# Optimization experiments

Hardware: AMD Instinct MI355X
Metric: run time of the kernel (lower is better)

## Reference

```python
import jax, jax.numpy as jnp
import numpy as np

N_CHANNELS = 1024
N_HEADS = 16
BLOCK_SIZE = 2048
BATCH = 4
SEQ = 2048


def setup_inputs() -> dict:
    key = jax.random.key(0)
    k_x, k_wqkv, k_wproj = jax.random.split(key, 3)
    x = jax.random.normal(k_x, (BATCH, SEQ, N_CHANNELS), dtype=jnp.float32)
    # torch nn.Linear: y = x @ W.T + b, W shape [out, in], init normal(std=0.02)
    W_qkv = jax.random.normal(k_wqkv, (3 * N_CHANNELS, N_CHANNELS), dtype=jnp.float32) * 0.02
    b_qkv = jnp.zeros((3 * N_CHANNELS,), dtype=jnp.float32)
    W_proj = jax.random.normal(k_wproj, (N_CHANNELS, N_CHANNELS), dtype=jnp.float32) * 0.02
    b_proj = jnp.zeros((N_CHANNELS,), dtype=jnp.float32)
    return {"x": x, "W_qkv": W_qkv, "b_qkv": b_qkv, "W_proj": W_proj, "b_proj": b_proj}


def reference(x, W_qkv, b_qkv, W_proj, b_proj):
    bs, n, n_channels = x.shape
    n_heads = N_HEADS
    head_dim = n_channels // n_heads
    scale = head_dim ** (-0.5)

    qkv = x @ W_qkv.T + b_qkv                              # [b, n, 3C]
    qkv = qkv.reshape(bs, n, 3, n_heads, head_dim)
    q, k, v = qkv[:, :, 0], qkv[:, :, 1], qkv[:, :, 2]     # [b, n, h, d]

    logits = jnp.einsum('bthc,bshc->bhts', q, k) * scale   # [b, h, t, s]
    # causal mask: log(tril(ones)) = 0 below diagonal, -inf above
    causal = jnp.tril(jnp.ones((n, n), dtype=bool))
    logits = jnp.where(causal[None, None], logits, -jnp.inf)
    attn = jax.nn.softmax(logits, axis=-1)

    output = jnp.einsum('bhts,bshc->bthc', attn, v)        # [b, t, h, d]
    output = output.reshape(bs, n, n_channels)
    output = output @ W_proj.T + b_proj
    return output
```

## Files before the change

kernel.cpp:

```cpp
#include <hip/hip_runtime.h>
#include <hip/hip_bf16.h>
#include <stdint.h>

#define BATCH 4
#define SEQ   2048
#define NC    1024
#define NH    16
#define HD    64
#define NT    16

typedef __bf16 bf16x8 __attribute__((ext_vector_type(8)));
typedef __bf16 bf16x2 __attribute__((ext_vector_type(2)));
typedef float  f32x4  __attribute__((ext_vector_type(4)));
typedef float  f32x16 __attribute__((ext_vector_type(16)));

#define DEV __device__ __forceinline__

DEV unsigned short f2bf(float f) {
    union { float f; unsigned u; } v; v.f = f;
    unsigned r = (v.u + 0x7fffu + ((v.u >> 16) & 1u)) >> 16;
    return (unsigned short)r;
}

DEV float fast_exp2(float x) {
#if __has_builtin(__builtin_amdgcn_exp2f)
    return __builtin_amdgcn_exp2f(x);
#else
    return exp2f(x);
#endif
}

DEV void plane32_swap(uint32_t& a, uint32_t& b) {
#if __has_builtin(__builtin_amdgcn_permlane32_swap)
    auto r = __builtin_amdgcn_permlane32_swap(a, b, false, false);
    a = (uint32_t)r[0];
    b = (uint32_t)r[1];
#else
    uint32_t sa = __shfl_xor(a, 32), sb = __shfl_xor(b, 32);
    const bool hi = ((threadIdx.x & 63) >= 32);
    uint32_t na = hi ? sb : a;
    uint32_t nb = hi ? b : sa;
    a = na; b = nb;
#endif
}

#define GLDS16(gsrc, ldst)                                                           \
    __builtin_amdgcn_global_load_lds(                                                \
        (const __attribute__((address_space(1))) unsigned int*)(gsrc),               \
        (__attribute__((address_space(3))) unsigned int*)(ldst), 16, 0, 0)

__global__ void cvt_kernel(const float* __restrict__ in, unsigned short* __restrict__ out, int n4) {
    int i = blockIdx.x * 256 + threadIdx.x;
    if (i >= n4) return;
    float4 v = reinterpret_cast<const float4*>(in)[i];
    ushort4 o;
    o.x = f2bf(v.x); o.y = f2bf(v.y); o.z = f2bf(v.z); o.w = f2bf(v.w);
    reinterpret_cast<ushort4*>(out)[i] = o;
}

template <bool BF16_OUT>
__global__ __launch_bounds__(256, 2) void gemm_bt_kernel(
    const unsigned short* __restrict__ A,
    const unsigned short* __restrict__ W,
    const float* __restrict__ bias,
    void* __restrict__ Cout,
    int M, int N, int K, int scale_n, float scale)
{
    __shared__ __align__(16) char Alds[128 * 128];
    __shared__ __align__(16) char Blds[128 * 128];

    const int tid = threadIdx.x;
    const int w = tid >> 6, l = tid & 63, g = l >> 4, lr = l & 15;
    const int nt = N >> 7;
    const int cpx = gridDim.x >> 3;
    const int bid = (blockIdx.x & 7) * cpx + (blockIdx.x >> 3);
    const int mtile = bid / nt, ntile = bid % nt;
    const int m0 = mtile << 7, n0 = ntile << 7;
    const int wr = (w >> 1) << 6, wc = (w & 1) << 6;

    f32x4 acc[4][4] = {};

    for (int kt = 0; kt < K; kt += 64) {
        if (kt) __syncthreads();
#pragma unroll
        for (int i = 0; i < 4; ++i) {
            const int issue = (i << 2) + w;
            const int row = (issue << 3) + (l >> 3);
            const int chunk = (l & 7) ^ (row & 7);
            GLDS16((const char*)(A + (size_t)(m0 + row) * K + kt) + (chunk << 4),
                   Alds + (issue << 10));
        }
#pragma unroll
        for (int i = 0; i < 4; ++i) {
            const int issue = (i << 2) + w;
            const int row = (issue << 3) + (l >> 3);
            const int chunk = (l & 7) ^ (row & 7);
            GLDS16((const char*)(W + (size_t)(n0 + row) * K + kt) + (chunk << 4),
                   Blds + (issue << 10));
        }
        __syncthreads();

#pragma unroll
        for (int kb = 0; kb < 2; ++kb) {
            bf16x8 af[4], bfr[4];
#pragma unroll
            for (int mf = 0; mf < 4; ++mf) {
                const int row = wr + (mf << 4) + lr;
                const int chunk = ((kb << 2) + g) ^ (row & 7);
                af[mf] = *reinterpret_cast<const bf16x8*>(Alds + row * 128 + (chunk << 4));
            }
#pragma unroll
            for (int nf = 0; nf < 4; ++nf) {
                const int row = wc + (nf << 4) + lr;
                const int chunk = ((kb << 2) + g) ^ (row & 7);
                bfr[nf] = *reinterpret_cast<const bf16x8*>(Blds + row * 128 + (chunk << 4));
            }
#pragma unroll
            for (int mf = 0; mf < 4; ++mf)
#pragma unroll
                for (int nf = 0; nf < 4; ++nf)
                    acc[mf][nf] = __builtin_amdgcn_mfma_f32_16x16x32_bf16(
                        af[mf], bfr[nf], acc[mf][nf], 0, 0, 0);
        }
    }

#pragma unroll
    for (int mf = 0; mf < 4; ++mf) {
#pragma unroll
        for (int nf = 0; nf < 4; ++nf) {
            const int n = n0 + wc + (nf << 4) + lr;
            const float bscale = (n < scale_n) ? scale : 1.0f;
            const float bv = bias[n];
#pragma unroll
            for (int r = 0; r < 4; ++r) {
                const int m = m0 + wr + (mf << 4) + (g << 2) + r;
                float v2 = (acc[mf][nf][r] + bv) * bscale;
                if (BF16_OUT)
                    ((unsigned short*)Cout)[(size_t)m * N + n] = f2bf(v2);
                else
                    ((float*)Cout)[(size_t)m * N + n] = v2;
            }
        }
    }
}

__global__ __launch_bounds__(256, 4) void attn_kernel(
    const unsigned short* __restrict__ qkv,
    unsigned short* __restrict__ ctx)
{
    __shared__ __align__(16) char Klds[2][8192];
    __shared__ __align__(16) char Vt[2][64 * 144];

    const int tid = threadIdx.x;
    const int w = tid >> 6, l = tid & 63, hi = l >> 5, lq = l & 31;
    const int bid = blockIdx.x;
    const int qt = NT - 1 - (bid >> 6);
    const int h = (bid >> 2) & 15, b = bid & 3;
    const unsigned short* base = qkv + (size_t)b * SEQ * 3072 + h * 64;

    const int vkey0 = (tid >> 5) << 3;
    const int vd0   = (tid & 31) << 1;
    const unsigned short* vbase = base + 2048 + (size_t)vkey0 * 3072 + vd0;

    const int q0 = (qt << 7) + (w << 5);
    const int q = q0 + lq;
    const int ntiles = (qt + 1) << 1;

    bf16x8 qfr[4];
#pragma unroll
    for (int ds = 0; ds < 4; ++ds)
        qfr[ds] = *reinterpret_cast<const bf16x8*>(
            base + (size_t)q * 3072 + (ds << 4) + (hi << 3));

    f32x16 acc0 = {}, acc1 = {};
    float mrun = -INFINITY, lrun = 0.f;

    uint32_t vreg[8];

#pragma unroll
    for (int i = 0; i < 8; ++i)
        vreg[i] = *reinterpret_cast<const uint32_t*>(vbase + (size_t)i * 3072);
#pragma unroll
    for (int i = 0; i < 2; ++i) {
        const int issue = (i << 2) + w;
        const int row = (issue << 3) + (l >> 3);
        const int chunk = (l & 7) ^ (row & 7);
        GLDS16((const char*)(base + 1024 + (size_t)row * 3072) + (chunk << 4),
               Klds[0] + (issue << 10));
    }
    {
        uint4 a, bq;
        a.x = (vreg[0] & 0xffffu) | (vreg[1] << 16);
        a.y = (vreg[2] & 0xffffu) | (vreg[3] << 16);
        a.z = (vreg[4] & 0xffffu) | (vreg[5] << 16);
        a.w = (vreg[6] & 0xffffu) | (vreg[7] << 16);
        bq.x = (vreg[0] >> 16) | (vreg[1] & 0xffff0000u);
        bq.y = (vreg[2] >> 16) | (vreg[3] & 0xffff0000u);
        bq.z = (vreg[4] >> 16) | (vreg[5] & 0xffff0000u);
        bq.w = (vreg[6] >> 16) | (vreg[7] & 0xffff0000u);
        *reinterpret_cast<uint4*>(Vt[0] + vd0 * 144 + vkey0 * 2) = a;
        *reinterpret_cast<uint4*>(Vt[0] + (vd0 + 1) * 144 + vkey0 * 2) = bq;
    }
    __syncthreads();

    for (int t = 0; t < ntiles; ++t) {
        const int cur = t & 1;
        const int kv0 = t << 6;
        const bool pf_ = (t + 1 < ntiles);

        if (pf_) {
            const int kv1 = kv0 + 64;
#pragma unroll
            for (int i = 0; i < 8; ++i)
                vreg[i] = *reinterpret_cast<const uint32_t*>(
                    vbase + (size_t)(kv1 + i) * 3072);
#pragma unroll
            for (int i = 0; i < 2; ++i) {
                const int issue = (i << 2) + w;
                const int row = (issue << 3) + (l >> 3);
                const int chunk = (l & 7) ^ (row & 7);
                GLDS16((const char*)(base + 1024 + (size_t)(kv1 + row) * 3072) + (chunk << 4),
                       Klds[cur ^ 1] + (issue << 10));
            }
        }

        if (kv0 <= q0 + 31) {
            const bool do1 = (kv0 + 32 <= q0 + 31);

            f32x16 st0 = {}, st1 = {};
#pragma unroll
            for (int ds = 0; ds < 4; ++ds) {
                const int chunk = (((ds << 1) + hi) ^ (lq & 7)) << 4;
                bf16x8 k0 = *reinterpret_cast<const bf16x8*>(
                    Klds[cur] + lq * 128 + chunk);
                st0 = __builtin_amdgcn_mfma_f32_32x32x16_bf16(k0, qfr[ds], st0, 0, 0, 0);
            }
            if (do1) {
#pragma unroll
                for (int ds = 0; ds < 4; ++ds) {
                    const int chunk = (((ds << 1) + hi) ^ (lq & 7)) << 4;
                    bf16x8 k1 = *reinterpret_cast<const bf16x8*>(
                        Klds[cur] + (lq + 32) * 128 + chunk);
                    st1 = __builtin_amdgcn_mfma_f32_32x32x16_bf16(k1, qfr[ds], st1, 0, 0, 0);
                }
            }

            if (kv0 + 31 > q0) {
#pragma unroll
                for (int r = 0; r < 16; ++r) {
                    const int key = kv0 + ((r & 3) + ((r >> 2) << 3) + (hi << 2));
                    if (key > q) st0[r] = -INFINITY;
                }
            }
            if (do1 && kv0 + 63 > q0) {
#pragma unroll
                for (int r = 0; r < 16; ++r) {
                    const int key = kv0 + 32 + ((r & 3) + ((r >> 2) << 3) + (hi << 2));
                    if (key > q) st1[r] = -INFINITY;
                }
            }

            float mt = st0[0];
#pragma unroll
            for (int r = 1; r < 16; ++r) mt = fmaxf(mt, st0[r]);
            if (do1) {
#pragma unroll
                for (int r = 0; r < 16; ++r) mt = fmaxf(mt, st1[r]);
            }
            mt = fmaxf(mt, __shfl_xor(mt, 32));
            if (__any(mt > mrun + 8.0f)) {
                const float mnew = fmaxf(mrun, mt);
                const float corr = fast_exp2(mrun - mnew);
                mrun = mnew;
                lrun *= corr;
#pragma unroll
                for (int r = 0; r < 16; ++r) { acc0[r] *= corr; acc1[r] *= corr; }
            }
            float rs = 0.f;
#pragma unroll
            for (int r = 0; r < 16; ++r) { st0[r] = fast_exp2(st0[r] - mrun); rs += st0[r]; }
            if (do1) {
#pragma unroll
                for (int r = 0; r < 16; ++r) { st1[r] = fast_exp2(st1[r] - mrun); rs += st1[r]; }
            }
            rs += __shfl_xor(rs, 32);
            lrun += rs;

            uint32_t pk0[8], pk1[8];
#pragma unroll
            for (int s = 0; s < 4; ++s)
#pragma unroll
                for (int c = 0; c < 2; ++c) {
                    bf16x2 t0 = {(__bf16)st0[(s << 2) + (c << 1)],
                                 (__bf16)st0[(s << 2) + (c << 1) + 1]};
                    pk0[(s << 1) + c] = __builtin_bit_cast(uint32_t, t0);
                }
            if (do1) {
#pragma unroll
                for (int s = 0; s < 4; ++s)
#pragma unroll
                    for (int c = 0; c < 2; ++c) {
                        bf16x2 t1 = {(__bf16)st1[(s << 2) + (c << 1)],
                                     (__bf16)st1[(s << 2) + (c << 1) + 1]};
                        pk1[(s << 1) + c] = __builtin_bit_cast(uint32_t, t1);
                    }
            }

            const int nkt = do1 ? 4 : 2;
#pragma unroll
            for (int kt = 0; kt < 4; ++kt) {
                if (kt >= nkt) break;
                const int s0 = (kt & 1) << 1;
                uint32_t x0, x1, y0, y1;
                if (kt < 2) {
                    x0 = pk0[(s0 << 1) + 0]; x1 = pk0[(s0 << 1) + 1];
                    y0 = pk0[(s0 << 1) + 2]; y1 = pk0[(s0 << 1) + 3];
                } else {
                    x0 = pk1[(s0 << 1) + 0]; x1 = pk1[(s0 << 1) + 1];
                    y0 = pk1[(s0 << 1) + 2]; y1 = pk1[(s0 << 1) + 3];
                }
                plane32_swap(x0, y0);
                plane32_swap(x1, y1);
                union { uint32_t u[4]; bf16x8 v; } pf;
                pf.u[0] = x0; pf.u[1] = x1; pf.u[2] = y0; pf.u[3] = y1;

                const char* vrow = Vt[cur] + ((kt << 4) + (hi << 3)) * 2;
                bf16x8 vf0 = *reinterpret_cast<const bf16x8*>(vrow + lq * 144);
                bf16x8 vf1 = *reinterpret_cast<const bf16x8*>(vrow + (lq + 32) * 144);
                acc0 = __builtin_amdgcn_mfma_f32_32x32x16_bf16(vf0, pf.v, acc0, 0, 0, 0);
                acc1 = __builtin_amdgcn_mfma_f32_32x32x16_bf16(vf1, pf.v, acc1, 0, 0, 0);
            }
        }

        if (pf_) {
            uint4 a, bq;
            a.x = (vreg[0] & 0xffffu) | (vreg[1] << 16);
            a.y = (vreg[2] & 0xffffu) | (vreg[3] << 16);
            a.z = (vreg[4] & 0xffffu) | (vreg[5] << 16);
            a.w = (vreg[6] & 0xffffu) | (vreg[7] << 16);
            bq.x = (vreg[0] >> 16) | (vreg[1] & 0xffff0000u);
            bq.y = (vreg[2] >> 16) | (vreg[3] & 0xffff0000u);
            bq.z = (vreg[4] >> 16) | (vreg[5] & 0xffff0000u);
            bq.w = (vreg[6] >> 16) | (vreg[7] & 0xffff0000u);
            char* vt = Vt[cur ^ 1];
            *reinterpret_cast<uint4*>(vt + vd0 * 144 + vkey0 * 2) = a;
            *reinterpret_cast<uint4*>(vt + (vd0 + 1) * 144 + vkey0 * 2) = bq;
            __syncthreads();
        }
    }

    {
        const float li = 1.0f / lrun;
        unsigned short* op = ctx + (size_t)(b * SEQ + q) * NC + h * HD;
#pragma unroll
        for (int r = 0; r < 16; ++r) {
            const int d = (r & 3) + ((r >> 2) << 3) + (hi << 2);
            op[d] = f2bf(acc0[r] * li);
            op[d + 32] = f2bf(acc1[r] * li);
        }
    }
}

extern "C" void kernel_launch(void* const* d_in, const int* in_sizes, int n_in,
                              void* d_out, int out_size, void* d_ws, size_t ws_size,
                              hipStream_t stream) {
    const float* x     = (const float*)d_in[0];
    const float* Wqkv  = (const float*)d_in[1];
    const float* bqkv  = (const float*)d_in[2];
    const float* Wproj = (const float*)d_in[3];
    const float* bproj = (const float*)d_in[4];
    float* out = (float*)d_out;

    const int M = BATCH * SEQ;
    unsigned short* ws = (unsigned short*)d_ws;
    unsigned short* xb     = ws;
    unsigned short* wqkvb  = xb + (size_t)M * NC;
    unsigned short* wprojb = wqkvb + (size_t)3 * NC * NC;
    unsigned short* qkvb   = wprojb + (size_t)NC * NC;
    unsigned short* ctxb   = qkvb + (size_t)M * 3 * NC;

    {
        int n4 = M * NC / 4;
        cvt_kernel<<<(n4 + 255) / 256, 256, 0, stream>>>(x, xb, n4);
    }
    {
        int n4 = 3 * NC * NC / 4;
        cvt_kernel<<<(n4 + 255) / 256, 256, 0, stream>>>(Wqkv, wqkvb, n4);
    }
    {
        int n4 = NC * NC / 4;
        cvt_kernel<<<(n4 + 255) / 256, 256, 0, stream>>>(Wproj, wprojb, n4);
    }

    gemm_bt_kernel<true><<<(M / 128) * (3 * NC / 128), 256, 0, stream>>>(
        xb, wqkvb, bqkv, qkvb, M, 3 * NC, NC, NC, 0.18033688011112042f);

    attn_kernel<<<NT * NH * BATCH, 256, 0, stream>>>(qkvb, ctxb);

    gemm_bt_kernel<false><<<(M / 128) * (NC / 128), 256, 0, stream>>>(
        ctxb, wprojb, bproj, out, M, NC, NC, 0, 1.0f);
}
```

Baseline: 158.8 us.

## Swizzle transposed V in LDS, snake query-tile order, add MFMA priority hints

The transposed V tile in LDS moves from a padded 144-byte row stride to a 128-byte stride with XOR swizzling of 16-byte chunks. This cuts LDS use and is meant to avoid bank conflicts on both the transpose writes and the MFMA operand reads. Block-to-query-tile mapping becomes a serpentine order across groups of four tiles, to balance causal work across waves of blocks. s_setprio raises wave priority around the QK and PV MFMA sections so matrix instructions issue ahead of other waves.

```diff
diff --git a/kernel.cpp b/kernel.cpp
--- a/kernel.cpp
+++ b/kernel.cpp
@@ -149,17 +149,20 @@
     unsigned short* __restrict__ ctx)
 {
     __shared__ __align__(16) char Klds[2][8192];
-    __shared__ __align__(16) char Vt[2][64 * 144];
+    __shared__ __align__(16) char Vt[2][8192];
 
     const int tid = threadIdx.x;
     const int w = tid >> 6, l = tid & 63, hi = l >> 5, lq = l & 31;
     const int bid = blockIdx.x;
-    const int qt = NT - 1 - (bid >> 6);
-    const int h = (bid >> 2) & 15, b = bid & 3;
+    const int s = bid >> 8, u = (bid >> 6) & 3, r0 = bid & 63;
+    const int v = (s & 1) ? 3 - u : u;
+    const int qt = NT - 1 - (s << 2) - v;
+    const int h = r0 >> 2, b = r0 & 3;
     const unsigned short* base = qkv + (size_t)b * SEQ * 3072 + h * 64;
 
     const int vkey0 = (tid >> 5) << 3;
     const int vd0   = (tid & 31) << 1;
+    const int vcc0  = vkey0 >> 3;
     const unsigned short* vbase = base + 2048 + (size_t)vkey0 * 3072 + vd0;
 
     const int q0 = (qt << 7) + (w << 5);
@@ -198,8 +201,10 @@
         bq.y = (vreg[2] >> 16) | (vreg[3] & 0xffff0000u);
         bq.z = (vreg[4] >> 16) | (vreg[5] & 0xffff0000u);
         bq.w = (vreg[6] >> 16) | (vreg[7] & 0xffff0000u);
-        *reinterpret_cast<uint4*>(Vt[0] + vd0 * 144 + vkey0 * 2) = a;
-        *reinterpret_cast<uint4*>(Vt[0] + (vd0 + 1) * 144 + vkey0 * 2) = bq;
+        *reinterpret_cast<uint4*>(
+            Vt[0] + vd0 * 128 + ((vcc0 ^ (vd0 & 7)) << 4)) = a;
+        *reinterpret_cast<uint4*>(
+            Vt[0] + (vd0 + 1) * 128 + ((vcc0 ^ ((vd0 + 1) & 7)) << 4)) = bq;
     }
     __syncthreads();
 
@@ -228,6 +233,7 @@
             const bool do1 = (kv0 + 32 <= q0 + 31);
 
             f32x16 st0 = {}, st1 = {};
+            __builtin_amdgcn_s_setprio(1);
 #pragma unroll
             for (int ds = 0; ds < 4; ++ds) {
                 const int chunk = (((ds << 1) + hi) ^ (lq & 7)) << 4;
@@ -244,6 +250,7 @@
                     st1 = __builtin_amdgcn_mfma_f32_32x32x16_bf16(k1, qfr[ds], st1, 0, 0, 0);
                 }
             }
+            __builtin_amdgcn_s_setprio(0);
 
             if (kv0 + 31 > q0) {
 #pragma unroll
@@ -288,25 +295,26 @@
 
             uint32_t pk0[8], pk1[8];
 #pragma unroll
-            for (int s = 0; s < 4; ++s)
+            for (int sp = 0; sp < 4; ++sp)
 #pragma unroll
                 for (int c = 0; c < 2; ++c) {
-                    bf16x2 t0 = {(__bf16)st0[(s << 2) + (c << 1)],
-                                 (__bf16)st0[(s << 2) + (c << 1) + 1]};
-                    pk0[(s << 1) + c] = __builtin_bit_cast(uint32_t, t0);
+                    bf16x2 t0 = {(__bf16)st0[(sp << 2) + (c << 1)],
+                                 (__bf16)st0[(sp << 2) + (c << 1) + 1]};
+                    pk0[(sp << 1) + c] = __builtin_bit_cast(uint32_t, t0);
                 }
             if (do1) {
 #pragma unroll
-                for (int s = 0; s < 4; ++s)
+                for (int sp = 0; sp < 4; ++sp)
 #pragma unroll
                     for (int c = 0; c < 2; ++c) {
-                        bf16x2 t1 = {(__bf16)st1[(s << 2) + (c << 1)],
-                                     (__bf16)st1[(s << 2) + (c << 1) + 1]};
-                        pk1[(s << 1) + c] = __builtin_bit_cast(uint32_t, t1);
+                        bf16x2 t1 = {(__bf16)st1[(sp << 2) + (c << 1)],
+                                     (__bf16)st1[(sp << 2) + (c << 1) + 1]};
+                        pk1[(sp << 1) + c] = __builtin_bit_cast(uint32_t, t1);
                     }
             }
 
             const int nkt = do1 ? 4 : 2;
+            __builtin_amdgcn_s_setprio(1);
 #pragma unroll
             for (int kt = 0; kt < 4; ++kt) {
                 if (kt >= nkt) break;
@@ -324,12 +332,16 @@
                 union { uint32_t u[4]; bf16x8 v; } pf;
                 pf.u[0] = x0; pf.u[1] = x1; pf.u[2] = y0; pf.u[3] = y1;
 
-                const char* vrow = Vt[cur] + ((kt << 4) + (hi << 3)) * 2;
-                bf16x8 vf0 = *reinterpret_cast<const bf16x8*>(vrow + lq * 144);
-                bf16x8 vf1 = *reinterpret_cast<const bf16x8*>(vrow + (lq + 32) * 144);
+                const int cc = (kt << 1) + hi;
+                const char* vt = Vt[cur];
+                bf16x8 vf0 = *reinterpret_cast<const bf16x8*>(
+                    vt + lq * 128 + ((cc ^ (lq & 7)) << 4));
+                bf16x8 vf1 = *reinterpret_cast<const bf16x8*>(
+                    vt + (lq + 32) * 128 + ((cc ^ (lq & 7)) << 4));
                 acc0 = __builtin_amdgcn_mfma_f32_32x32x16_bf16(vf0, pf.v, acc0, 0, 0, 0);
                 acc1 = __builtin_amdgcn_mfma_f32_32x32x16_bf16(vf1, pf.v, acc1, 0, 0, 0);
             }
+            __builtin_amdgcn_s_setprio(0);
         }
 
         if (pf_) {
@@ -343,8 +355,10 @@
             bq.z = (vreg[4] >> 16) | (vreg[5] & 0xffff0000u);
             bq.w = (vreg[6] >> 16) | (vreg[7] & 0xffff0000u);
             char* vt = Vt[cur ^ 1];
-            *reinterpret_cast<uint4*>(vt + vd0 * 144 + vkey0 * 2) = a;
-            *reinterpret_cast<uint4*>(vt + (vd0 + 1) * 144 + vkey0 * 2) = bq;
+            *reinterpret_cast<uint4*>(
+                vt + vd0 * 128 + ((vcc0 ^ (vd0 & 7)) << 4)) = a;
+            *reinterpret_cast<uint4*>(
+                vt + (vd0 + 1) * 128 + ((vcc0 ^ ((vd0 + 1) & 7)) << 4)) = bq;
             __syncthreads();
         }
     }
```

New measurement: 160.2 us. About the same (+0.9%).
